# Kernel optimization log

Hardware: AMD Instinct MI355X
Metric: run time of the kernel (lower is better)

## Reference

```python
import jax, jax.numpy as jnp
import numpy as np

INPUT_SIZE = 512
HIDDEN_SIZE = 512
BATCH = 32
SEQ = 2048


def setup_inputs() -> dict:
    key = jax.random.key(0)
    keys = jax.random.split(key, 17)
    stdv = 1.0 / np.sqrt(HIDDEN_SIZE)

    def u(k, shape):
        return jax.random.uniform(k, shape, jnp.float32, -stdv, stdv)

    H, I = HIDDEN_SIZE, INPUT_SIZE
    inp = {"inputs": jax.random.normal(keys[0], (BATCH, SEQ, I), jnp.float32)}
    names = [("w_ii", (H, I)), ("w_hi", (H, H)), ("b_ii", (H, 1)), ("b_hi", (H, 1)),
             ("w_if", (H, I)), ("w_hf", (H, H)), ("b_if", (H, 1)), ("b_hf", (H, 1)),
             ("w_io", (H, I)), ("w_ho", (H, H)), ("b_io", (H, 1)), ("b_ho", (H, 1)),
             ("w_ig", (H, I)), ("w_hg", (H, H)), ("b_ig", (H, 1)), ("b_hg", (H, 1))]
    for k, (name, shape) in zip(keys[1:], names):
        inp[name] = u(k, shape)
    return inp


def reference(inputs, w_ii, w_hi, b_ii, b_hi, w_if, w_hf, b_if, b_hf,
              w_io, w_ho, b_io, b_ho, w_ig, w_hg, b_ig, b_hg):
    # inputs: [B, S, I] -> scan over time. State h,c: [B, H].
    B, S, _ = inputs.shape
    H = w_ii.shape[0]
    # Stack the 4 gate weights so each step is one input GEMM + one recurrent GEMM.
    Wx = jnp.concatenate([w_ii, w_if, w_ig, w_io], axis=0)      # [4H, I]
    Wh = jnp.concatenate([w_hi, w_hf, w_hg, w_ho], axis=0)      # [4H, H]
    b = jnp.concatenate([b_ii + b_hi, b_if + b_hf, b_ig + b_hg, b_io + b_ho], axis=0)[:, 0]  # [4H]

    # Precompute input contributions for all timesteps: [S, B, 4H]
    x_proj = jnp.einsum('bsi,gi->sbg', inputs, Wx) + b

    def step(carry, xp):
        h, c = carry                                  # [B, H]
        gates = xp + h @ Wh.T                         # [B, 4H]
        i, f, g, o = jnp.split(gates, 4, axis=-1)
        i = jax.nn.sigmoid(i)
        f = jax.nn.sigmoid(f)
        g = jnp.tanh(g)
        o = jax.nn.sigmoid(o)
        c_next = f * c + i * g
        h_next = o * jnp.tanh(c_next)
        return (h_next, c_next), h_next

    h0 = jnp.zeros((B, H), inputs.dtype)
    c0 = jnp.zeros((B, H), inputs.dtype)
    (h_last, c_last), hidden_seq = jax.lax.scan(step, (h0, c0), x_proj)
    # hidden_seq: [S, B, H] matches torch cat of [1, B, H] along dim 0
    return hidden_seq, (h_last[None], c_last[None])
```

## Files before the change

kernel.cpp:

```cpp
#include <hip/hip_runtime.h>

#define BATCH 32
#define SEQ   2048
#define ISZ   512
#define HSZ   512
#define GRID  256
#define TPB   512
#define SPIN_CAP 2000000

typedef unsigned long long u64;
typedef unsigned int u32;


__device__ __forceinline__ u64 ld_agent_u64(const u64* p) {
    return __hip_atomic_load(p, __ATOMIC_RELAXED, __HIP_MEMORY_SCOPE_AGENT);
}
__device__ __forceinline__ u32 ld_agent_u32(const u32* p) {
    return __hip_atomic_load(p, __ATOMIC_RELAXED, __HIP_MEMORY_SCOPE_AGENT);
}
__device__ __forceinline__ void st_agent_u32(u32* p, u32 v) {
    __hip_atomic_store(p, v, __ATOMIC_RELAXED, __HIP_MEMORY_SCOPE_AGENT);
}
__device__ __forceinline__ void st_agent_f32(float* p, float v) {
    __hip_atomic_store(p, v, __ATOMIC_RELAXED, __HIP_MEMORY_SCOPE_AGENT);
}
__device__ __forceinline__ float u2f(u32 u) { union { u32 u; float f; } c; c.u = u; return c.f; }

__global__ __launch_bounds__(TPB)
void lstm_persistent(const float* __restrict__ inp,
                     const float* __restrict__ w_ii, const float* __restrict__ w_hi,
                     const float* __restrict__ b_ii, const float* __restrict__ b_hi,
                     const float* __restrict__ w_if, const float* __restrict__ w_hf,
                     const float* __restrict__ b_if, const float* __restrict__ b_hf,
                     const float* __restrict__ w_io, const float* __restrict__ w_ho,
                     const float* __restrict__ b_io, const float* __restrict__ b_ho,
                     const float* __restrict__ w_ig, const float* __restrict__ w_hg,
                     const float* __restrict__ b_ig, const float* __restrict__ b_hg,
                     float* __restrict__ out, u32* __restrict__ beac)
{
    __shared__ float lh[8 * 512];
    __shared__ float gpre[32][9];
    __shared__ float lbias[32];

    const int tid = threadIdx.x;
    const int g   = blockIdx.x;
    const int bg  = g & 3;
    const int b0  = bg * 8;
    const int p   = g >> 2;
    const int d0  = p * 8;

    const int rp = tid >> 5;
    const int ks = tid & 31;
    const int r0 = 2 * rp;
    const int gg = r0 >> 3;
    const int dl0 = r0 & 7, dl1 = dl0 + 1;
    const int xr  = (ks >> 1) & 7;
    const int bb = tid >> 6;
    const int cc = tid & 63;

    const float* whp[4] = { w_hi, w_hf, w_hg, w_ho };
    const float* wxp[4] = { w_ii, w_if, w_ig, w_io };
    const float* bip[4] = { b_ii, b_if, b_ig, b_io };
    const float* bhp[4] = { b_hi, b_hf, b_hg, b_ho };

    if (tid < 32) {
        int g2 = tid >> 3, d2 = tid & 7;
        lbias[tid] = bip[g2][d0 + d2] + bhp[g2][d0 + d2];
    }

    float4 wx0[4], wx1[4], wh0[4], wh1[4];
    {
        const float* x0 = wxp[gg] + (size_t)(d0 + dl0) * 512 + ks * 16;
        const float* x1 = wxp[gg] + (size_t)(d0 + dl1) * 512 + ks * 16;
        const float* h0 = whp[gg] + (size_t)(d0 + dl0) * 512 + ks * 16;
        const float* h1 = whp[gg] + (size_t)(d0 + dl1) * 512 + ks * 16;
        #pragma unroll
        for (int j = 0; j < 4; ++j) {
            wx0[j] = *(const float4*)(x0 + 4 * j);
            wx1[j] = *(const float4*)(x1 + 4 * j);
            wh0[j] = *(const float4*)(h0 + 4 * j);
            wh1[j] = *(const float4*)(h1 + 4 * j);
        }
    }
    __syncthreads();

    float xpc0[8], xpc1[8], xpn0[8], xpn1[8];

    auto xproj = [&](int tt, int blo, int bhi, float* q0, float* q1) {
        for (int b = blo; b < bhi; ++b) {
            const float* src = inp + ((size_t)(b0 + b) * SEQ + tt) * ISZ + ks * 16;
            float4 o0 = *(const float4*)(src);
            float4 o1 = *(const float4*)(src + 4);
            float4 o2 = *(const float4*)(src + 8);
            float4 o3 = *(const float4*)(src + 12);
            float a0 = 0.f, a1 = 0.f;
            a0 = fmaf(wx0[0].x,o0.x,a0); a0 = fmaf(wx0[0].y,o0.y,a0); a0 = fmaf(wx0[0].z,o0.z,a0); a0 = fmaf(wx0[0].w,o0.w,a0);
            a0 = fmaf(wx0[1].x,o1.x,a0); a0 = fmaf(wx0[1].y,o1.y,a0); a0 = fmaf(wx0[1].z,o1.z,a0); a0 = fmaf(wx0[1].w,o1.w,a0);
            a0 = fmaf(wx0[2].x,o2.x,a0); a0 = fmaf(wx0[2].y,o2.y,a0); a0 = fmaf(wx0[2].z,o2.z,a0); a0 = fmaf(wx0[2].w,o2.w,a0);
            a0 = fmaf(wx0[3].x,o3.x,a0); a0 = fmaf(wx0[3].y,o3.y,a0); a0 = fmaf(wx0[3].z,o3.z,a0); a0 = fmaf(wx0[3].w,o3.w,a0);
            a1 = fmaf(wx1[0].x,o0.x,a1); a1 = fmaf(wx1[0].y,o0.y,a1); a1 = fmaf(wx1[0].z,o0.z,a1); a1 = fmaf(wx1[0].w,o0.w,a1);
            a1 = fmaf(wx1[1].x,o1.x,a1); a1 = fmaf(wx1[1].y,o1.y,a1); a1 = fmaf(wx1[1].z,o1.z,a1); a1 = fmaf(wx1[1].w,o1.w,a1);
            a1 = fmaf(wx1[2].x,o2.x,a1); a1 = fmaf(wx1[2].y,o2.y,a1); a1 = fmaf(wx1[2].z,o2.z,a1); a1 = fmaf(wx1[2].w,o2.w,a1);
            a1 = fmaf(wx1[3].x,o3.x,a1); a1 = fmaf(wx1[3].y,o3.y,a1); a1 = fmaf(wx1[3].z,o3.z,a1); a1 = fmaf(wx1[3].w,o3.w,a1);
            q0[b] = a0; q1[b] = a1;
        }
    };

    xproj(0, 0, 8, xpc0, xpc1);

    float h_keep = 0.f, c_keep = 0.f, c_reg = 0.f;

    for (int t = 0; t < SEQ; ++t) {
        if (t + 1 < SEQ) xproj(t + 1, 0, 4, xpn0, xpn1);

        if (t > 0) {
            if (tid < 64) {
                const u32 tt = (u32)t;
                const u32* bp = beac + bg * 64 + tid;
                u32 v = ld_agent_u32(bp);
                int spin = 0;
                while (v < tt) {
                    __builtin_amdgcn_s_sleep(1);
                    v = ld_agent_u32(bp);
                    if (++spin > SPIN_CAP) break;
                }
            }
            __syncthreads();

            const u64* src64 = (const u64*)(out + (size_t)(t - 1) * BATCH * HSZ
                                                + (size_t)(b0 + bb) * HSZ + cc * 8);
            u64 v0 = ld_agent_u64(src64 + 0);
            u64 v1 = ld_agent_u64(src64 + 1);
            u64 v2 = ld_agent_u64(src64 + 2);
            u64 v3 = ld_agent_u64(src64 + 3);

            if (t + 1 < SEQ) xproj(t + 1, 4, 8, xpn0, xpn1);

            float4 wA, wB;
            wA.x = u2f((u32)v0); wA.y = u2f((u32)(v0 >> 32));
            wA.z = u2f((u32)v1); wA.w = u2f((u32)(v1 >> 32));
            wB.x = u2f((u32)v2); wB.y = u2f((u32)(v2 >> 32));
            wB.z = u2f((u32)v3); wB.w = u2f((u32)(v3 >> 32));
            const int qA = 2 * cc, qB = 2 * cc + 1;
            *(float4*)(&lh[bb * 512 + (qA ^ ((qA >> 3) & 7)) * 4]) = wA;
            *(float4*)(&lh[bb * 512 + (qB ^ ((qB >> 3) & 7)) * 4]) = wB;
            __syncthreads();
        } else {
            if (t + 1 < SEQ) xproj(t + 1, 4, 8, xpn0, xpn1);
        }

        #pragma unroll
        for (int b = 0; b < 8; ++b) {
            float a0 = xpc0[b], a1 = xpc1[b];
            if (t > 0) {
                const float* hb = &lh[b * 512];
                float4 o0 = *(const float4*)(hb + ((4 * ks + 0) ^ xr) * 4);
                float4 o1 = *(const float4*)(hb + ((4 * ks + 1) ^ xr) * 4);
                float4 o2 = *(const float4*)(hb + ((4 * ks + 2) ^ xr) * 4);
                float4 o3 = *(const float4*)(hb + ((4 * ks + 3) ^ xr) * 4);
                a0 = fmaf(wh0[0].x,o0.x,a0); a0 = fmaf(wh0[0].y,o0.y,a0); a0 = fmaf(wh0[0].z,o0.z,a0); a0 = fmaf(wh0[0].w,o0.w,a0);
                a0 = fmaf(wh0[1].x,o1.x,a0); a0 = fmaf(wh0[1].y,o1.y,a0); a0 = fmaf(wh0[1].z,o1.z,a0); a0 = fmaf(wh0[1].w,o1.w,a0);
                a0 = fmaf(wh0[2].x,o2.x,a0); a0 = fmaf(wh0[2].y,o2.y,a0); a0 = fmaf(wh0[2].z,o2.z,a0); a0 = fmaf(wh0[2].w,o2.w,a0);
                a0 = fmaf(wh0[3].x,o3.x,a0); a0 = fmaf(wh0[3].y,o3.y,a0); a0 = fmaf(wh0[3].z,o3.z,a0); a0 = fmaf(wh0[3].w,o3.w,a0);
                a1 = fmaf(wh1[0].x,o0.x,a1); a1 = fmaf(wh1[0].y,o0.y,a1); a1 = fmaf(wh1[0].z,o0.z,a1); a1 = fmaf(wh1[0].w,o0.w,a1);
                a1 = fmaf(wh1[1].x,o1.x,a1); a1 = fmaf(wh1[1].y,o1.y,a1); a1 = fmaf(wh1[1].z,o1.z,a1); a1 = fmaf(wh1[1].w,o1.w,a1);
                a1 = fmaf(wh1[2].x,o2.x,a1); a1 = fmaf(wh1[2].y,o2.y,a1); a1 = fmaf(wh1[2].z,o2.z,a1); a1 = fmaf(wh1[2].w,o2.w,a1);
                a1 = fmaf(wh1[3].x,o3.x,a1); a1 = fmaf(wh1[3].y,o3.y,a1); a1 = fmaf(wh1[3].z,o3.z,a1); a1 = fmaf(wh1[3].w,o3.w,a1);
            }
            #pragma unroll
            for (int m = 16; m >= 1; m >>= 1) {
                a0 += __shfl_xor(a0, m);
                a1 += __shfl_xor(a1, m);
            }
            if ((tid & 31) == 0) {
                gpre[r0][b]     = a0;
                gpre[r0 + 1][b] = a1;
            }
        }
        __syncthreads();

        if (tid < 64) {
            int b = tid >> 3, dl = tid & 7;
            float iv = gpre[0  + dl][b] + lbias[0  + dl];
            float fv = gpre[8  + dl][b] + lbias[8  + dl];
            float gv = gpre[16 + dl][b] + lbias[16 + dl];
            float ov = gpre[24 + dl][b] + lbias[24 + dl];
            iv = 1.f / (1.f + __expf(-iv));
            fv = 1.f / (1.f + __expf(-fv));
            gv = tanhf(gv);
            ov = 1.f / (1.f + __expf(-ov));
            float c = fv * c_reg + iv * gv;
            float h = ov * tanhf(c);
            c_reg = c; h_keep = h; c_keep = c;
            st_agent_f32(out + (size_t)t * BATCH * HSZ + (size_t)(b0 + b) * HSZ + (d0 + dl), h);
            if (t + 1 < SEQ) {
                asm volatile("s_waitcnt vmcnt(0)" ::: "memory");
                if (tid == 0) st_agent_u32(beac + bg * 64 + p, (u32)(t + 1));
            }
        }

        #pragma unroll
        for (int b = 0; b < 8; ++b) { xpc0[b] = xpn0[b]; xpc1[b] = xpn1[b]; }
    }

    if (tid < 64) {
        int b = tid >> 3, dl = tid & 7;
        size_t base = (size_t)SEQ * BATCH * HSZ;
        out[base + (size_t)(b0 + b) * HSZ + (d0 + dl)] = h_keep;
        out[base + (size_t)BATCH * HSZ + (size_t)(b0 + b) * HSZ + (d0 + dl)] = c_keep;
    }
}

extern "C" void kernel_launch(void* const* d_in, const int* in_sizes, int n_in,
                              void* d_out, int out_size, void* d_ws, size_t ws_size,
                              hipStream_t stream) {
    const float* inp  = (const float*)d_in[0];
    const float* w_ii = (const float*)d_in[1];
    const float* w_hi = (const float*)d_in[2];
    const float* b_ii = (const float*)d_in[3];
    const float* b_hi = (const float*)d_in[4];
    const float* w_if = (const float*)d_in[5];
    const float* w_hf = (const float*)d_in[6];
    const float* b_if = (const float*)d_in[7];
    const float* b_hf = (const float*)d_in[8];
    const float* w_io = (const float*)d_in[9];
    const float* w_ho = (const float*)d_in[10];
    const float* b_io = (const float*)d_in[11];
    const float* b_ho = (const float*)d_in[12];
    const float* w_ig = (const float*)d_in[13];
    const float* w_hg = (const float*)d_in[14];
    const float* b_ig = (const float*)d_in[15];
    const float* b_hg = (const float*)d_in[16];
    float* out = (float*)d_out;
    u32* beac = (u32*)d_ws;

    hipMemsetAsync(d_ws, 0, 4096, stream);

    void* args[] = { (void*)&inp,
                     (void*)&w_ii, (void*)&w_hi, (void*)&b_ii, (void*)&b_hi,
                     (void*)&w_if, (void*)&w_hf, (void*)&b_if, (void*)&b_hf,
                     (void*)&w_io, (void*)&w_ho, (void*)&b_io, (void*)&b_ho,
                     (void*)&w_ig, (void*)&w_hg, (void*)&b_ig, (void*)&b_hg,
                     (void*)&out, (void*)&beac };
    hipError_t err = hipLaunchCooperativeKernel((const void*)lstm_persistent,
                                                dim3(GRID), dim3(TPB), args, 0, stream);
    if (err != hipSuccess) {
        lstm_persistent<<<dim3(GRID), dim3(TPB), 0, stream>>>(
            inp, w_ii, w_hi, b_ii, b_hi, w_if, w_hf, b_if, b_hf,
            w_io, w_ho, b_io, b_ho, w_ig, w_hg, b_ig, b_hg, out, beac);
    }
}
```

Baseline: 16.41 ms.

## Replace per-step beacon flags with canary-polled hidden-state data

Drops the per-block beacon counters and their store/wait handshake. Instead the output buffer is prefilled with a NaN canary value, and each thread spins directly on its own slice of the previous timestep's h until no canary remains. The first half of the next-step input projection is moved to overlap with that first load. This removes a flag round-trip and an s_waitcnt/store per step. In exchange it adds a full memset of the 128 MB output buffer on every launch, and it relies on h never equalling the canary bit pattern.

```diff
diff --git a/kernel.cpp b/kernel.cpp
--- a/kernel.cpp
+++ b/kernel.cpp
@@ -7,6 +7,7 @@
 #define GRID  256
 #define TPB   512
 #define SPIN_CAP 2000000
+#define CANARY 0x7fc0deadu
 
 typedef unsigned long long u64;
 typedef unsigned int u32;
@@ -15,16 +16,13 @@
 __device__ __forceinline__ u64 ld_agent_u64(const u64* p) {
     return __hip_atomic_load(p, __ATOMIC_RELAXED, __HIP_MEMORY_SCOPE_AGENT);
 }
-__device__ __forceinline__ u32 ld_agent_u32(const u32* p) {
-    return __hip_atomic_load(p, __ATOMIC_RELAXED, __HIP_MEMORY_SCOPE_AGENT);
-}
-__device__ __forceinline__ void st_agent_u32(u32* p, u32 v) {
-    __hip_atomic_store(p, v, __ATOMIC_RELAXED, __HIP_MEMORY_SCOPE_AGENT);
-}
 __device__ __forceinline__ void st_agent_f32(float* p, float v) {
     __hip_atomic_store(p, v, __ATOMIC_RELAXED, __HIP_MEMORY_SCOPE_AGENT);
 }
 __device__ __forceinline__ float u2f(u32 u) { union { u32 u; float f; } c; c.u = u; return c.f; }
+__device__ __forceinline__ int ok64(u64 v) {
+    return ((u32)v != CANARY) & ((u32)(v >> 32) != CANARY);
+}
 
 __global__ __launch_bounds__(TPB)
 void lstm_persistent(const float* __restrict__ inp,
@@ -111,28 +109,25 @@
     float h_keep = 0.f, c_keep = 0.f, c_reg = 0.f;
 
     for (int t = 0; t < SEQ; ++t) {
-        if (t + 1 < SEQ) xproj(t + 1, 0, 4, xpn0, xpn1);
-
         if (t > 0) {
-            if (tid < 64) {
-                const u32 tt = (u32)t;
-                const u32* bp = beac + bg * 64 + tid;
-                u32 v = ld_agent_u32(bp);
-                int spin = 0;
-                while (v < tt) {
-                    __builtin_amdgcn_s_sleep(1);
-                    v = ld_agent_u32(bp);
-                    if (++spin > SPIN_CAP) break;
-                }
-            }
-            __syncthreads();
-
             const u64* src64 = (const u64*)(out + (size_t)(t - 1) * BATCH * HSZ
                                                 + (size_t)(b0 + bb) * HSZ + cc * 8);
             u64 v0 = ld_agent_u64(src64 + 0);
             u64 v1 = ld_agent_u64(src64 + 1);
             u64 v2 = ld_agent_u64(src64 + 2);
             u64 v3 = ld_agent_u64(src64 + 3);
+
+            if (t + 1 < SEQ) xproj(t + 1, 0, 4, xpn0, xpn1);
+
+            int spin = 0;
+            while (!(ok64(v0) & ok64(v1) & ok64(v2) & ok64(v3))) {
+                __builtin_amdgcn_s_sleep(1);
+                v0 = ld_agent_u64(src64 + 0);
+                v1 = ld_agent_u64(src64 + 1);
+                v2 = ld_agent_u64(src64 + 2);
+                v3 = ld_agent_u64(src64 + 3);
+                if (++spin > SPIN_CAP) break;
+            }
 
             if (t + 1 < SEQ) xproj(t + 1, 4, 8, xpn0, xpn1);
 
@@ -146,7 +141,7 @@
             *(float4*)(&lh[bb * 512 + (qB ^ ((qB >> 3) & 7)) * 4]) = wB;
             __syncthreads();
         } else {
-            if (t + 1 < SEQ) xproj(t + 1, 4, 8, xpn0, xpn1);
+            if (t + 1 < SEQ) { xproj(t + 1, 0, 4, xpn0, xpn1); xproj(t + 1, 4, 8, xpn0, xpn1); }
         }
 
         #pragma unroll
@@ -193,10 +188,6 @@
             float h = ov * tanhf(c);
             c_reg = c; h_keep = h; c_keep = c;
             st_agent_f32(out + (size_t)t * BATCH * HSZ + (size_t)(b0 + b) * HSZ + (d0 + dl), h);
-            if (t + 1 < SEQ) {
-                asm volatile("s_waitcnt vmcnt(0)" ::: "memory");
-                if (tid == 0) st_agent_u32(beac + bg * 64 + p, (u32)(t + 1));
-            }
         }
 
         #pragma unroll
@@ -234,7 +225,8 @@
     float* out = (float*)d_out;
     u32* beac = (u32*)d_ws;
 
-    hipMemsetAsync(d_ws, 0, 4096, stream);
+    hipMemsetD32Async((hipDeviceptr_t)out, (int)CANARY,
+                      (size_t)SEQ * BATCH * HSZ, stream);
 
     void* args[] = { (void*)&inp,
                      (void*)&w_ii, (void*)&w_hi, (void*)&b_ii, (void*)&b_hi,
```

Measured after the change: 18.47 ms. 1.13x slower.

## Repartition LSTM work into 8 batch groups of 4 with 32 producers each

Applied to the files above, without the earlier changes.

Changes the block decomposition from 4 batch groups of 8 rows (64 blocks per group) to 8 batch groups of 4 rows (32 blocks per group), each block now owning 16 hidden units with 1024 threads. Each block waits on fewer producer beacons and loads a smaller h slice per step, shrinking per-step synchronisation fan-in and the recurrent data each block must gather. It also merges the separate post-load barrier into the one before the gate computation. In exchange, each block keeps twice as many weights in registers across more threads, which may lower occupancy and cause register pressure or spilling at 1024 threads per block.

```diff
diff --git a/kernel.cpp b/kernel.cpp
--- a/kernel.cpp
+++ b/kernel.cpp
@@ -5,26 +5,31 @@
 #define ISZ   512
 #define HSZ   512
 #define GRID  256
-#define TPB   512
+#define TPB   1024
+#define NB    4
+#define NPROD 32
+#define ND    16
 #define SPIN_CAP 2000000
 
+typedef unsigned int u32;
 typedef unsigned long long u64;
-typedef unsigned int u32;
-
-
-__device__ __forceinline__ u64 ld_agent_u64(const u64* p) {
+
+
+__device__ __forceinline__ float u2f(u32 u){ union{u32 u; float f;}c; c.u=u; return c.f; }
+__device__ __forceinline__ u32 f2u(float f){ union{float f; u32 u;}c; c.f=f; return c.u; }
+
+__device__ __forceinline__ u32 ld_agent_u32(const u32* p){
     return __hip_atomic_load(p, __ATOMIC_RELAXED, __HIP_MEMORY_SCOPE_AGENT);
 }
-__device__ __forceinline__ u32 ld_agent_u32(const u32* p) {
+__device__ __forceinline__ u64 ld_agent_u64(const u64* p){
     return __hip_atomic_load(p, __ATOMIC_RELAXED, __HIP_MEMORY_SCOPE_AGENT);
 }
-__device__ __forceinline__ void st_agent_u32(u32* p, u32 v) {
+__device__ __forceinline__ void st_agent_u32(u32* p, u32 v){
     __hip_atomic_store(p, v, __ATOMIC_RELAXED, __HIP_MEMORY_SCOPE_AGENT);
 }
-__device__ __forceinline__ void st_agent_f32(float* p, float v) {
+__device__ __forceinline__ void st_agent_f32(float* p, float v){
     __hip_atomic_store(p, v, __ATOMIC_RELAXED, __HIP_MEMORY_SCOPE_AGENT);
 }
-__device__ __forceinline__ float u2f(u32 u) { union { u32 u; float f; } c; c.u = u; return c.f; }
 
 __global__ __launch_bounds__(TPB)
 void lstm_persistent(const float* __restrict__ inp,
@@ -36,44 +41,45 @@
                      const float* __restrict__ b_io, const float* __restrict__ b_ho,
                      const float* __restrict__ w_ig, const float* __restrict__ w_hg,
                      const float* __restrict__ b_ig, const float* __restrict__ b_hg,
-                     float* __restrict__ out, u32* __restrict__ beac)
+                     float* __restrict__ out, u32* __restrict__ ws)
 {
-    __shared__ float lh[8 * 512];
-    __shared__ float gpre[32][9];
-    __shared__ float lbias[32];
+    __shared__ float lh[NB * HSZ];
+    __shared__ float gpre[64][5];
+    __shared__ float lbias[64];
 
     const int tid = threadIdx.x;
     const int g   = blockIdx.x;
-    const int bg  = g & 3;
-    const int b0  = bg * 8;
-    const int p   = g >> 2;
-    const int d0  = p * 8;
+
+    const int grp  = g >> 5;
+    const int rank = g & 31;
+    const int B4 = grp * NB;
+    const int d0 = rank * ND;
 
     const int rp = tid >> 5;
     const int ks = tid & 31;
     const int r0 = 2 * rp;
-    const int gg = r0 >> 3;
-    const int dl0 = r0 & 7, dl1 = dl0 + 1;
+    const int gg = r0 >> 4;
+    const int dl0 = r0 & 15, dl1 = dl0 + 1;
     const int xr  = (ks >> 1) & 7;
-    const int bb = tid >> 6;
-    const int cc = tid & 63;
+    const int bt = tid >> 7;
+    const int cc = tid & 127;
 
     const float* whp[4] = { w_hi, w_hf, w_hg, w_ho };
     const float* wxp[4] = { w_ii, w_if, w_ig, w_io };
     const float* bip[4] = { b_ii, b_if, b_ig, b_io };
     const float* bhp[4] = { b_hi, b_hf, b_hg, b_ho };
 
-    if (tid < 32) {
-        int g2 = tid >> 3, d2 = tid & 7;
+    if (tid < 64) {
+        int g2 = tid >> 4, d2 = tid & 15;
         lbias[tid] = bip[g2][d0 + d2] + bhp[g2][d0 + d2];
     }
 
     float4 wx0[4], wx1[4], wh0[4], wh1[4];
     {
-        const float* x0 = wxp[gg] + (size_t)(d0 + dl0) * 512 + ks * 16;
-        const float* x1 = wxp[gg] + (size_t)(d0 + dl1) * 512 + ks * 16;
-        const float* h0 = whp[gg] + (size_t)(d0 + dl0) * 512 + ks * 16;
-        const float* h1 = whp[gg] + (size_t)(d0 + dl1) * 512 + ks * 16;
+        const float* x0 = wxp[gg] + (size_t)(d0 + dl0) * HSZ + ks * 16;
+        const float* x1 = wxp[gg] + (size_t)(d0 + dl1) * HSZ + ks * 16;
+        const float* h0 = whp[gg] + (size_t)(d0 + dl0) * HSZ + ks * 16;
+        const float* h1 = whp[gg] + (size_t)(d0 + dl1) * HSZ + ks * 16;
         #pragma unroll
         for (int j = 0; j < 4; ++j) {
             wx0[j] = *(const float4*)(x0 + 4 * j);
@@ -84,11 +90,11 @@
     }
     __syncthreads();
 
-    float xpc0[8], xpc1[8], xpn0[8], xpn1[8];
+    float xpc0[4], xpc1[4], xpn0[4], xpn1[4];
 
     auto xproj = [&](int tt, int blo, int bhi, float* q0, float* q1) {
         for (int b = blo; b < bhi; ++b) {
-            const float* src = inp + ((size_t)(b0 + b) * SEQ + tt) * ISZ + ks * 16;
+            const float* src = inp + ((size_t)(B4 + b) * SEQ + tt) * ISZ + ks * 16;
             float4 o0 = *(const float4*)(src);
             float4 o1 = *(const float4*)(src + 4);
             float4 o2 = *(const float4*)(src + 8);
@@ -106,51 +112,50 @@
         }
     };
 
-    xproj(0, 0, 8, xpc0, xpc1);
+    xproj(0, 0, 4, xpc0, xpc1);
 
     float h_keep = 0.f, c_keep = 0.f, c_reg = 0.f;
 
     for (int t = 0; t < SEQ; ++t) {
-        if (t + 1 < SEQ) xproj(t + 1, 0, 4, xpn0, xpn1);
-
         if (t > 0) {
-            if (tid < 64) {
-                const u32 tt = (u32)t;
-                const u32* bp = beac + bg * 64 + tid;
-                u32 v = ld_agent_u32(bp);
+            if (t + 1 < SEQ) xproj(t + 1, 0, 2, xpn0, xpn1);
+
+            if (tid < NPROD) {
+                const u32* bp = ws + grp * NPROD + tid;
+                u32 bv = ld_agent_u32(bp);
                 int spin = 0;
-                while (v < tt) {
+                while (bv < (u32)t) {
                     __builtin_amdgcn_s_sleep(1);
-                    v = ld_agent_u32(bp);
+                    bv = ld_agent_u32(bp);
                     if (++spin > SPIN_CAP) break;
                 }
             }
             __syncthreads();
 
-            const u64* src64 = (const u64*)(out + (size_t)(t - 1) * BATCH * HSZ
-                                                + (size_t)(b0 + bb) * HSZ + cc * 8);
-            u64 v0 = ld_agent_u64(src64 + 0);
-            u64 v1 = ld_agent_u64(src64 + 1);
-            u64 v2 = ld_agent_u64(src64 + 2);
-            u64 v3 = ld_agent_u64(src64 + 3);
-
-            if (t + 1 < SEQ) xproj(t + 1, 4, 8, xpn0, xpn1);
-
-            float4 wA, wB;
-            wA.x = u2f((u32)v0); wA.y = u2f((u32)(v0 >> 32));
-            wA.z = u2f((u32)v1); wA.w = u2f((u32)(v1 >> 32));
-            wB.x = u2f((u32)v2); wB.y = u2f((u32)(v2 >> 32));
-            wB.z = u2f((u32)v3); wB.w = u2f((u32)(v3 >> 32));
-            const int qA = 2 * cc, qB = 2 * cc + 1;
-            *(float4*)(&lh[bb * 512 + (qA ^ ((qA >> 3) & 7)) * 4]) = wA;
-            *(float4*)(&lh[bb * 512 + (qB ^ ((qB >> 3) & 7)) * 4]) = wB;
-            __syncthreads();
+            u64 v0 = 0, v1 = 0;
+            if (tid < 512) {
+                const u64* src = (const u64*)(out + (size_t)(t - 1) * BATCH * HSZ
+                                                  + (size_t)(B4 + bt) * HSZ + cc * 4);
+                v0 = ld_agent_u64(src);
+                v1 = ld_agent_u64(src + 1);
+            }
+
+            if (t + 1 < SEQ) xproj(t + 1, 2, 4, xpn0, xpn1);
+
+            if (tid < 512) {
+                float4 w;
+                w.x = u2f((u32)v0); w.y = u2f((u32)(v0 >> 32));
+                w.z = u2f((u32)v1); w.w = u2f((u32)(v1 >> 32));
+                const int qs = cc ^ ((cc >> 3) & 7);
+                *(float4*)(&lh[bt * 512 + qs * 4]) = w;
+            }
         } else {
-            if (t + 1 < SEQ) xproj(t + 1, 4, 8, xpn0, xpn1);
-        }
+            xproj(1, 0, 4, xpn0, xpn1);
+        }
+        __syncthreads();
 
         #pragma unroll
-        for (int b = 0; b < 8; ++b) {
+        for (int b = 0; b < 4; ++b) {
             float a0 = xpc0[b], a1 = xpc1[b];
             if (t > 0) {
                 const float* hb = &lh[b * 512];
@@ -180,11 +185,11 @@
         __syncthreads();
 
         if (tid < 64) {
-            int b = tid >> 3, dl = tid & 7;
+            int b = tid >> 4, dl = tid & 15;
             float iv = gpre[0  + dl][b] + lbias[0  + dl];
-            float fv = gpre[8  + dl][b] + lbias[8  + dl];
-            float gv = gpre[16 + dl][b] + lbias[16 + dl];
-            float ov = gpre[24 + dl][b] + lbias[24 + dl];
+            float fv = gpre[16 + dl][b] + lbias[16 + dl];
+            float gv = gpre[32 + dl][b] + lbias[32 + dl];
+            float ov = gpre[48 + dl][b] + lbias[48 + dl];
             iv = 1.f / (1.f + __expf(-iv));
             fv = 1.f / (1.f + __expf(-fv));
             gv = tanhf(gv);
@@ -192,22 +197,22 @@
             float c = fv * c_reg + iv * gv;
             float h = ov * tanhf(c);
             c_reg = c; h_keep = h; c_keep = c;
-            st_agent_f32(out + (size_t)t * BATCH * HSZ + (size_t)(b0 + b) * HSZ + (d0 + dl), h);
+            st_agent_f32(out + (size_t)t * BATCH * HSZ + (size_t)(B4 + b) * HSZ + (d0 + dl), h);
             if (t + 1 < SEQ) {
                 asm volatile("s_waitcnt vmcnt(0)" ::: "memory");
-                if (tid == 0) st_agent_u32(beac + bg * 64 + p, (u32)(t + 1));
+                if (tid == 0) st_agent_u32(ws + grp * NPROD + rank, (u32)(t + 1));
             }
         }
 
         #pragma unroll
-        for (int b = 0; b < 8; ++b) { xpc0[b] = xpn0[b]; xpc1[b] = xpn1[b]; }
+        for (int b = 0; b < 4; ++b) { xpc0[b] = xpn0[b]; xpc1[b] = xpn1[b]; }
     }
 
     if (tid < 64) {
-        int b = tid >> 3, dl = tid & 7;
+        int b = tid >> 4, dl = tid & 15;
         size_t base = (size_t)SEQ * BATCH * HSZ;
-        out[base + (size_t)(b0 + b) * HSZ + (d0 + dl)] = h_keep;
-        out[base + (size_t)BATCH * HSZ + (size_t)(b0 + b) * HSZ + (d0 + dl)] = c_keep;
+        out[base + (size_t)(B4 + b) * HSZ + (d0 + dl)] = h_keep;
+        out[base + (size_t)BATCH * HSZ + (size_t)(B4 + b) * HSZ + (d0 + dl)] = c_keep;
     }
 }
 
@@ -232,7 +237,7 @@
     const float* b_ig = (const float*)d_in[15];
     const float* b_hg = (const float*)d_in[16];
     float* out = (float*)d_out;
-    u32* beac = (u32*)d_ws;
+    u32* ws = (u32*)d_ws;
 
     hipMemsetAsync(d_ws, 0, 4096, stream);
 
@@ -241,12 +246,12 @@
                      (void*)&w_if, (void*)&w_hf, (void*)&b_if, (void*)&b_hf,
                      (void*)&w_io, (void*)&w_ho, (void*)&b_io, (void*)&b_ho,
                      (void*)&w_ig, (void*)&w_hg, (void*)&b_ig, (void*)&b_hg,
-                     (void*)&out, (void*)&beac };
+                     (void*)&out, (void*)&ws };
     hipError_t err = hipLaunchCooperativeKernel((const void*)lstm_persistent,
                                                 dim3(GRID), dim3(TPB), args, 0, stream);
     if (err != hipSuccess) {
         lstm_persistent<<<dim3(GRID), dim3(TPB), 0, stream>>>(
             inp, w_ii, w_hi, b_ii, b_hi, w_if, w_hf, b_if, b_hf,
-            w_io, w_ho, b_io, b_ho, w_ig, w_hg, b_ig, b_hg, out, beac);
-    }
-}
+            w_io, w_ho, b_io, b_ho, w_ig, w_hg, b_ig, b_hg, out, ws);
+    }
+}
```

Result: slower. 58.07 ms (+253.8%).
